# Kernel optimization log

Measured on AMD Instinct MI355X. Metric: run time of the kernel, lower is better.

Reference implementation:

```python
import jax, jax.numpy as jnp
import numpy as np
from jax import lax

EPS = 1e-5
NEG_SLOPE = 0.2


def inorm(x):
    # InstanceNorm3d (affine=False): per-sample, per-channel over spatial dims
    m = x.mean(axis=(2, 3, 4), keepdims=True)
    v = x.var(axis=(2, 3, 4), keepdims=True)
    return (x - m) * lax.rsqrt(v + EPS)


def lrelu(x):
    return jax.nn.leaky_relu(x, NEG_SLOPE)


def conv3d(x, w, b, pad, reflect=False):
    if pad > 0:
        mode = 'reflect' if reflect else 'constant'
        x = jnp.pad(x, ((0, 0), (0, 0), (pad, pad), (pad, pad), (pad, pad)), mode=mode)
    y = lax.conv_general_dilated(x, w, (1, 1, 1), 'VALID',
                                 dimension_numbers=('NCDHW', 'OIDHW', 'NCDHW'))
    return y + b[None, :, None, None, None]


def conv_block(x, w, b, pad):
    # ConvBlock: InstanceNorm -> LeakyReLU(0.2) -> Conv3d (reflect padding)
    return conv3d(lrelu(inorm(x)), w, b, pad, reflect=True)


def deform_conv3d(x, offset, w):
    # 3D deformable convolution, k=3, stride=1, pad=1, trilinear sampling, no bias
    B, C, H, W, D = x.shape
    K3 = 27
    off = offset.reshape(B, K3, 3, H, W, D)
    t = jnp.arange(3) - 1  # kernel taps relative to center (pad=1)
    tz, ty, tx = jnp.meshgrid(t, t, t, indexing='ij')
    taps = jnp.stack([tz, ty, tx], axis=-1).reshape(K3, 3).astype(x.dtype)
    gz, gy, gx = jnp.meshgrid(jnp.arange(H), jnp.arange(W), jnp.arange(D), indexing='ij')
    grid = jnp.stack([gz, gy, gx]).astype(x.dtype)  # [3,H,W,D]
    # sampling positions: [B,K3,3,H,W,D]
    pos = grid[None, None] + taps[None, :, :, None, None, None] + off
    p0 = jnp.floor(pos)
    frac = pos - p0
    p0i = p0.astype(jnp.int32)
    dims = jnp.array([H, W, D], dtype=jnp.int32)[None, None, :, None, None, None]
    xf = x.reshape(B, C, H * W * D)
    acc = jnp.zeros((B, C, K3, H * W * D), x.dtype)
    for dz in (0, 1):
        for dy in (0, 1):
            for dx in (0, 1):
                d = jnp.array([dz, dy, dx], dtype=jnp.int32)[None, None, :, None, None, None]
                idx = p0i + d  # [B,K3,3,H,W,D]
                valid = jnp.all((idx >= 0) & (idx < dims), axis=2)  # zero outside
                w3 = jnp.where(d == 1, frac, 1.0 - frac)
                wgt = w3.prod(axis=2) * valid.astype(x.dtype)  # [B,K3,H,W,D]
                ic = jnp.clip(idx, 0, dims - 1)
                flat = ((ic[:, :, 0] * W + ic[:, :, 1]) * D + ic[:, :, 2]).reshape(B, K3, -1)
                vals = jax.vmap(lambda xb, ib: xb[:, ib])(xf, flat)  # [B,C,K3,HWD]
                acc = acc + vals * wgt.reshape(B, 1, K3, -1)
    out = jnp.einsum('oik,bikp->bop', w.reshape(w.shape[0], w.shape[1], K3), acc)
    return out.reshape(B, -1, H, W, D)


def reference(x, w_first, b_first, w_na, b_na, w_last, b_last,
              w_fc1, b_fc1, w_fc2, b_fc2, w_off, b_off, w_def):
    B = x.shape[0]
    # SE-style channel-gated branch weights
    s = x.mean(axis=(2, 3, 4))                      # global avg pool -> [B,C]
    h = lrelu(s @ w_fc1.T + b_fc1)
    dw = jax.nn.softmax(h @ w_fc2.T + b_fc2, axis=1)  # [B,2]
    f = conv_block(x, w_first, b_first, pad=0)        # 1x1x1: 64 -> 32
    off = conv3d(f, w_off, b_off, pad=1, reflect=False)  # offsets [B,81,H,W,D]
    belta = deform_conv3d(f, off, w_def)
    alpha = conv_block(f, w_na, b_na, pad=1)
    comb = (belta * dw[:, 0][:, None, None, None, None]
            + alpha * dw[:, 1][:, None, None, None, None])
    return conv_block(comb, w_last, b_last, pad=0)


def setup_inputs() -> dict:
    key = jax.random.key(0)
    ks = jax.random.split(key, 16)
    C_in, C = 64, 32
    S = 32
    def rn(k, shape, scale):
        return jax.random.normal(k, shape, dtype=jnp.float32) * scale
    return {
        'x': rn(ks[0], (2, C_in, S, S, S), 1.0),
        'w_first': rn(ks[1], (C, C_in, 1, 1, 1), 0.05),
        'b_first': rn(ks[2], (C,), 0.05),
        'w_na': rn(ks[3], (C, C, 3, 3, 3), 0.05),
        'b_na': rn(ks[4], (C,), 0.05),
        'w_last': rn(ks[5], (C, C, 1, 1, 1), 0.05),
        'b_last': rn(ks[6], (C,), 0.05),
        'w_fc1': rn(ks[7], (16, C_in), 0.05),
        'b_fc1': rn(ks[8], (16,), 0.05),
        'w_fc2': rn(ks[9], (2, 16), 0.05),
        'b_fc2': rn(ks[10], (2,), 0.05),
        'w_off': rn(ks[11], (81, C, 3, 3, 3), 0.01),
        'b_off': jnp.zeros((81,), jnp.float32),
        'w_def': rn(ks[12], (C, C, 3, 3, 3), 0.05),
    }
```

## Files before the change

### kernel.cpp

```cpp
#include <hip/hip_runtime.h>
#include <hip/hip_bf16.h>

#define EPS 1e-5f

__global__ __launch_bounds__(256) void stats_kernel(
    const float* __restrict__ buf, float* __restrict__ mean,
    float* __restrict__ rstd) {
  int bc = blockIdx.x;
  const float* ch = buf + (size_t)bc * 32768;
  float s = 0.f, ss = 0.f;
  for (int i = threadIdx.x; i < 32768; i += 256) {
    float v = ch[i];
    s += v; ss += v * v;
  }
  for (int o = 32; o; o >>= 1) {
    s += __shfl_down(s, o);
    ss += __shfl_down(ss, o);
  }
  __shared__ float sb[4], ssb[4];
  int wid = threadIdx.x >> 6, lane = threadIdx.x & 63;
  if (lane == 0) { sb[wid] = s; ssb[wid] = ss; }
  __syncthreads();
  if (threadIdx.x == 0) {
    float S = 0.f, SS = 0.f;
    for (int w = 0; w < 4; ++w) { S += sb[w]; SS += ssb[w]; }
    float m = S * (1.f / 32768.f);
    float var = SS * (1.f / 32768.f) - m * m;
    mean[bc] = m;
    rstd[bc] = rsqrtf(var + EPS);
  }
}

__global__ void se_kernel(const float* __restrict__ mean_x,
                          const float* __restrict__ w1, const float* __restrict__ b1,
                          const float* __restrict__ w2, const float* __restrict__ b2,
                          float* __restrict__ dw) {
  __shared__ float hbuf[32];
  int t = threadIdx.x;
  if (t < 32) {
    int b = t >> 4, j = t & 15;
    float a = b1[j];
    for (int c = 0; c < 64; ++c) a += mean_x[b * 64 + c] * w1[j * 64 + c];
    hbuf[t] = a >= 0.f ? a : 0.2f * a;
  }
  __syncthreads();
  if (t < 2) {
    int b = t;
    float l0 = b2[0], l1 = b2[1];
    for (int j = 0; j < 16; ++j) {
      float h = hbuf[b * 16 + j];
      l0 += h * w2[j];
      l1 += h * w2[16 + j];
    }
    float m = fmaxf(l0, l1);
    float e0 = __expf(l0 - m), e1 = __expf(l1 - m);
    float inv = 1.f / (e0 + e1);
    dw[b * 2 + 0] = e0 * inv;
    dw[b * 2 + 1] = e1 * inv;
  }
}

__global__ __launch_bounds__(256) void prep_wdef(const float* __restrict__ w_def,
                                                 float* __restrict__ wTd) {
  int idx = blockIdx.x * 256 + threadIdx.x;
  if (idx < 27648) {
    int o = idx & 31, rest = idx >> 5;
    int i = rest & 31, k = rest >> 5;
    wTd[idx] = w_def[(size_t)(o * 32 + i) * 27 + k];
  }
}

__global__ __launch_bounds__(256) void prep_woff(const float* __restrict__ w_off,
                                                 float* __restrict__ wT) {
  int idx = blockIdx.x * 256 + threadIdx.x;
  if (idx < 69984) {
    int o = idx % 81, rest = idx / 81;
    int i = rest & 31, t = rest >> 5;
    wT[idx] = w_off[(size_t)(o * 32 + i) * 27 + t];
  }
}

__global__ __launch_bounds__(256) void prep_wna(const float* __restrict__ w_na,
                                                float* __restrict__ wT) {
  int idx = blockIdx.x * 256 + threadIdx.x;
  if (idx < 27648) {
    int o = idx & 31, rest = idx >> 5;
    int i = rest & 31, t = rest >> 5;
    wT[idx] = w_na[(size_t)(o * 32 + i) * 27 + t];
  }
}

__global__ __launch_bounds__(256) void first_conv_kernel(
    const float* __restrict__ x, const float* __restrict__ w,
    const float* __restrict__ bias,
    const float* __restrict__ meanp, const float* __restrict__ rstdp,
    float* __restrict__ f_cp, float* __restrict__ f_pc) {
  int og = blockIdx.x >> 8;
  int chunk = blockIdx.x & 255;
  int vg = chunk * 256 + threadIdx.x;
  int b = vg >> 15, p = vg & 32767;
  float acc[8];
#pragma unroll
  for (int o = 0; o < 8; ++o) acc[o] = 0.f;
  const float* xb = x + ((size_t)b * 64) * 32768;
  const float* wg = w + (size_t)og * 8 * 64;
  for (int i = 0; i < 64; ++i) {
    float v = xb[(size_t)i * 32768 + p];
    float m = meanp[b * 64 + i], r = rstdp[b * 64 + i];
    v = (v - m) * r;
    v = v >= 0.f ? v : 0.2f * v;
#pragma unroll
    for (int o = 0; o < 8; ++o) acc[o] = fmaf(wg[o * 64 + i], v, acc[o]);
  }
#pragma unroll
  for (int o = 0; o < 8; ++o) {
    acc[o] += bias[og * 8 + o];
    f_cp[((size_t)b * 32 + og * 8 + o) * 32768 + p] = acc[o];
  }
  float4 v0 = make_float4(acc[0], acc[1], acc[2], acc[3]);
  float4 v1 = make_float4(acc[4], acc[5], acc[6], acc[7]);
  float* pc = f_pc + ((size_t)b * 32768 + p) * 32 + og * 8;
  *(float4*)pc = v0;
  *(float4*)(pc + 4) = v1;
}

__global__ __launch_bounds__(256) void norm_f_kernel(
    const float* __restrict__ f_cp, const float* __restrict__ meanp,
    const float* __restrict__ rstdp, float* __restrict__ f_norm) {
  int i4 = blockIdx.x * 256 + threadIdx.x;
  int bc = (i4 * 4) >> 15;
  float m = meanp[bc], r = rstdp[bc];
  float4 v = ((const float4*)f_cp)[i4];
  float4 o;
  o.x = (v.x - m) * r; o.x = o.x >= 0.f ? o.x : 0.2f * o.x;
  o.y = (v.y - m) * r; o.y = o.y >= 0.f ? o.y : 0.2f * o.y;
  o.z = (v.z - m) * r; o.z = o.z >= 0.f ? o.z : 0.2f * o.z;
  o.w = (v.w - m) * r; o.w = o.w >= 0.f ? o.w : 0.2f * o.w;
  ((float4*)f_norm)[i4] = o;
}

template <int OCG, int OCT, bool REFLECT>
__global__ __launch_bounds__(256) void conv3_direct_kernel(
    const float* __restrict__ in,
    const float* __restrict__ wT,
    const float* __restrict__ bias,
    float* __restrict__ out) {
  int og = blockIdx.x >> 8;
  int chunk = blockIdx.x & 255;
  int vg = chunk * 256 + threadIdx.x;
  int b = vg >> 15, p = vg & 32767;
  int z = p >> 10, y = (p >> 5) & 31, x = p & 31;
  const float* base = in + ((size_t)b * 32) * 32768;

  float acc[OCG];
#pragma unroll
  for (int o = 0; o < OCG; ++o) acc[o] = 0.f;

  for (int t = 0; t < 27; ++t) {
    int dz = t / 9, dy = (t / 3) % 3, dx = t % 3;
    int zz = z + dz - 1, yy = y + dy - 1, xx = x + dx - 1;
    bool valid = true;
    if (REFLECT) {
      zz = zz < 0 ? -zz : (zz > 31 ? 62 - zz : zz);
      yy = yy < 0 ? -yy : (yy > 31 ? 62 - yy : yy);
      xx = xx < 0 ? -xx : (xx > 31 ? 62 - xx : xx);
    } else {
      valid = (unsigned)zz < 32u && (unsigned)yy < 32u && (unsigned)xx < 32u;
      if (!valid) { zz = 0; yy = 0; xx = 0; }
    }
    int off = (zz * 32 + yy) * 32 + xx;
    const float* cptr = base + off;
    const float* wt = wT + (size_t)t * 32 * OCT + og * OCG;
#pragma unroll 4
    for (int i = 0; i < 32; ++i) {
      float v = cptr[(size_t)i << 15];
      if (!REFLECT) v = valid ? v : 0.f;
#pragma unroll
      for (int o = 0; o < OCG; ++o)
        acc[o] = fmaf(wt[i * OCT + o], v, acc[o]);
    }
  }
  float* op = out + ((size_t)b * OCT + og * OCG) * 32768 + p;
#pragma unroll
  for (int o = 0; o < OCG; ++o)
    op[(size_t)o * 32768] = acc[o] + bias[og * OCG + o];
}

__global__ __launch_bounds__(256) void deform_kernel(
    const float* __restrict__ f_pc,
    const float* __restrict__ offs,
    const float* __restrict__ wTd,
    float* __restrict__ part) {
  int bid = blockIdx.x;
  int kg = bid >> 8;
  int tile = bid & 255;
  int vg = tile * 256 + threadIdx.x;
  int b = vg >> 15, p = vg & 32767;
  int z = p >> 10, y = (p >> 5) & 31, x = p & 31;
  const float* fb = f_pc + (((size_t)b) << 15) * 32;
  const float* ob = offs + (((size_t)b * 81) << 15);
  int kz = kg - 1;

  float acc[32];
#pragma unroll
  for (int o = 0; o < 32; ++o) acc[o] = 0.f;

  for (int kk = 0; kk < 9; ++kk) {
    int k = kg * 9 + kk;
    int ky = kk / 3 - 1, kx = kk % 3 - 1;

    float oz = ob[(size_t)(k * 3 + 0) * 32768 + p];
    float oy = ob[(size_t)(k * 3 + 1) * 32768 + p];
    float ox = ob[(size_t)(k * 3 + 2) * 32768 + p];
    float pz = (float)(z + kz) + oz;
    float py = (float)(y + ky) + oy;
    float px = (float)(x + kx) + ox;
    float fz = floorf(pz), fy = floorf(py), fxx = floorf(px);
    int iz0 = (int)fz, iy0 = (int)fy, ix0 = (int)fxx;
    float rz = pz - fz, ry = py - fy, rx = px - fxx;

    float v[32];
#pragma unroll
    for (int c = 0; c < 32; ++c) v[c] = 0.f;
#pragma unroll
    for (int corner = 0; corner < 8; ++corner) {
      int dz = corner >> 2, dy = (corner >> 1) & 1, dxx = corner & 1;
      int iz = iz0 + dz, iy = iy0 + dy, ix = ix0 + dxx;
      bool okb = (unsigned)iz < 32u && (unsigned)iy < 32u && (unsigned)ix < 32u;
      float wt = (dz ? rz : 1.f - rz) * (dy ? ry : 1.f - ry) *
                 (dxx ? rx : 1.f - rx);
      if (okb) {
        const float4* src =
            (const float4*)(fb + (size_t)((iz * 32 + iy) * 32 + ix) * 32);
#pragma unroll
        for (int q = 0; q < 8; ++q) {
          float4 u = src[q];
          v[q * 4 + 0] = fmaf(wt, u.x, v[q * 4 + 0]);
          v[q * 4 + 1] = fmaf(wt, u.y, v[q * 4 + 1]);
          v[q * 4 + 2] = fmaf(wt, u.z, v[q * 4 + 2]);
          v[q * 4 + 3] = fmaf(wt, u.w, v[q * 4 + 3]);
        }
      }
    }
    const float* wk = wTd + (size_t)k * 1024;
#pragma unroll
    for (int i = 0; i < 32; ++i) {
      float vi = v[i];
      const float* wr = wk + i * 32;
#pragma unroll
      for (int o = 0; o < 32; ++o) acc[o] = fmaf(wr[o], vi, acc[o]);
    }
  }
  float* obp = part + (((size_t)kg * 2 + b) * 32) * 32768 + p;
#pragma unroll
  for (int o = 0; o < 32; ++o) obp[(size_t)o * 32768] = acc[o];
}

__global__ __launch_bounds__(256) void combine_kernel(
    const float* __restrict__ part, const float* __restrict__ alpha,
    const float* __restrict__ dw, float* __restrict__ comb,
    float* __restrict__ partial) {
  int blk = blockIdx.x;
  int bc = blk >> 2, qt = blk & 3;
  int b = bc >> 5;
  float d0 = dw[b * 2 + 0], d1 = dw[b * 2 + 1];
  const float* p0 = part + (size_t)(bc) * 32768;
  const float* p1 = part + (size_t)(64 + bc) * 32768;
  const float* p2 = part + (size_t)(128 + bc) * 32768;
  const float* al = alpha + (size_t)bc * 32768;
  float* cb = comb + (size_t)bc * 32768;
  float s = 0.f, ss = 0.f;
  int i0 = qt * 8192;
  for (int i = i0 + threadIdx.x; i < i0 + 8192; i += 256) {
    float v = d0 * (p0[i] + p1[i] + p2[i]) + d1 * al[i];
    cb[i] = v;
    s += v; ss += v * v;
  }
  for (int o = 32; o; o >>= 1) {
    s += __shfl_down(s, o);
    ss += __shfl_down(ss, o);
  }
  __shared__ float sb[4], ssb[4];
  int wid = threadIdx.x >> 6, lane = threadIdx.x & 63;
  if (lane == 0) { sb[wid] = s; ssb[wid] = ss; }
  __syncthreads();
  if (threadIdx.x == 0) {
    float S = 0.f, SS = 0.f;
    for (int w = 0; w < 4; ++w) { S += sb[w]; SS += ssb[w]; }
    partial[blk * 2 + 0] = S;
    partial[blk * 2 + 1] = SS;
  }
}

__global__ void finalize_kernel(const float* __restrict__ partial,
                                float* __restrict__ mean, float* __restrict__ rstd) {
  int t = threadIdx.x;
  if (t < 64) {
    float S = 0.f, SS = 0.f;
    for (int q = 0; q < 4; ++q) {
      S += partial[(t * 4 + q) * 2 + 0];
      SS += partial[(t * 4 + q) * 2 + 1];
    }
    float m = S * (1.f / 32768.f);
    float var = SS * (1.f / 32768.f) - m * m;
    mean[t] = m;
    rstd[t] = rsqrtf(var + EPS);
  }
}

__global__ __launch_bounds__(256) void last_conv_kernel(
    const float* __restrict__ comb, const float* __restrict__ w,
    const float* __restrict__ bias,
    const float* __restrict__ meanp, const float* __restrict__ rstdp,
    float* __restrict__ out) {
  int og = blockIdx.x >> 8;
  int chunk = blockIdx.x & 255;
  int vg = chunk * 256 + threadIdx.x;
  int b = vg >> 15, p = vg & 32767;
  float acc[8];
#pragma unroll
  for (int o = 0; o < 8; ++o) acc[o] = 0.f;
  const float* cb = comb + ((size_t)b * 32) * 32768;
  const float* wg = w + (size_t)og * 8 * 32;
  for (int i = 0; i < 32; ++i) {
    float v = cb[(size_t)i * 32768 + p];
    float m = meanp[b * 32 + i], r = rstdp[b * 32 + i];
    v = (v - m) * r;
    v = v >= 0.f ? v : 0.2f * v;
#pragma unroll
    for (int o = 0; o < 8; ++o) acc[o] = fmaf(wg[o * 32 + i], v, acc[o]);
  }
#pragma unroll
  for (int o = 0; o < 8; ++o)
    out[((size_t)b * 32 + og * 8 + o) * 32768 + p] = acc[o] + bias[og * 8 + o];
}

extern "C" void kernel_launch(void* const* d_in, const int* in_sizes, int n_in,
                              void* d_out, int out_size, void* d_ws, size_t ws_size,
                              hipStream_t stream) {
  (void)in_sizes; (void)n_in; (void)out_size; (void)ws_size;
  const float* x       = (const float*)d_in[0];
  const float* w_first = (const float*)d_in[1];
  const float* b_first = (const float*)d_in[2];
  const float* w_na    = (const float*)d_in[3];
  const float* b_na    = (const float*)d_in[4];
  const float* w_last  = (const float*)d_in[5];
  const float* b_last  = (const float*)d_in[6];
  const float* w_fc1   = (const float*)d_in[7];
  const float* b_fc1   = (const float*)d_in[8];
  const float* w_fc2   = (const float*)d_in[9];
  const float* b_fc2   = (const float*)d_in[10];
  const float* w_off   = (const float*)d_in[11];
  const float* b_off   = (const float*)d_in[12];
  const float* w_def   = (const float*)d_in[13];
  float* out = (float*)d_out;

  float* ws = (float*)d_ws;
  float* mean_x  = ws + 0;
  float* rstd_x  = ws + 128;
  float* dwp     = ws + 256;
  float* mean_f  = ws + 272;
  float* rstd_f  = ws + 336;
  float* mean_c  = ws + 400;
  float* rstd_c  = ws + 464;
  float* partial = ws + 528;
  size_t off0 = 2048;
  float* wTd    = ws + off0;
  float* wT_off = wTd + 28672;
  float* wT_na  = wT_off + 71680;
  float* f_cp   = wT_na + 28672;
  float* f_pc   = f_cp + 2097152;
  float* offb   = f_pc + 2097152;
  float* alpha  = offb + 5308416;
  float* part   = alpha + 2097152;
  float* comb   = part + 6291456;
  float* f_norm = part;

  hipLaunchKernelGGL(stats_kernel, dim3(128), dim3(256), 0, stream, x, mean_x, rstd_x);
  hipLaunchKernelGGL(prep_wdef, dim3(108), dim3(256), 0, stream, w_def, wTd);
  hipLaunchKernelGGL(prep_woff, dim3(274), dim3(256), 0, stream, w_off, wT_off);
  hipLaunchKernelGGL(prep_wna, dim3(108), dim3(256), 0, stream, w_na, wT_na);
  hipLaunchKernelGGL(se_kernel, dim3(1), dim3(64), 0, stream,
                     mean_x, w_fc1, b_fc1, w_fc2, b_fc2, dwp);
  hipLaunchKernelGGL(first_conv_kernel, dim3(1024), dim3(256), 0, stream,
                     x, w_first, b_first, mean_x, rstd_x, f_cp, f_pc);
  hipLaunchKernelGGL(stats_kernel, dim3(64), dim3(256), 0, stream, f_cp, mean_f, rstd_f);
  hipLaunchKernelGGL(norm_f_kernel, dim3(2048), dim3(256), 0, stream,
                     f_cp, mean_f, rstd_f, f_norm);
  hipLaunchKernelGGL((conv3_direct_kernel<9, 81, false>), dim3(2304), dim3(256), 0, stream,
                     f_cp, wT_off, b_off, offb);
  hipLaunchKernelGGL((conv3_direct_kernel<8, 32, true>), dim3(1024), dim3(256), 0, stream,
                     f_norm, wT_na, b_na, alpha);
  hipLaunchKernelGGL(deform_kernel, dim3(768), dim3(256), 0, stream,
                     f_pc, offb, wTd, part);
  hipLaunchKernelGGL(combine_kernel, dim3(256), dim3(256), 0, stream,
                     part, alpha, dwp, comb, partial);
  hipLaunchKernelGGL(finalize_kernel, dim3(1), dim3(64), 0, stream,
                     partial, mean_c, rstd_c);
  hipLaunchKernelGGL(last_conv_kernel, dim3(1024), dim3(256), 0, stream,
                     comb, w_last, b_last, mean_c, rstd_c, out);
}
```

Measured before the change: 623.1 us.

## Gather deformable samples from channel-major features, dropping the point-major copy

```diff
diff --git a/kernel.cpp b/kernel.cpp
--- a/kernel.cpp
+++ b/kernel.cpp
@@ -94,7 +94,7 @@
     const float* __restrict__ x, const float* __restrict__ w,
     const float* __restrict__ bias,
     const float* __restrict__ meanp, const float* __restrict__ rstdp,
-    float* __restrict__ f_cp, float* __restrict__ f_pc) {
+    float* __restrict__ f_cp) {
   int og = blockIdx.x >> 8;
   int chunk = blockIdx.x & 255;
   int vg = chunk * 256 + threadIdx.x;
@@ -113,15 +113,8 @@
     for (int o = 0; o < 8; ++o) acc[o] = fmaf(wg[o * 64 + i], v, acc[o]);
   }
 #pragma unroll
-  for (int o = 0; o < 8; ++o) {
-    acc[o] += bias[og * 8 + o];
-    f_cp[((size_t)b * 32 + og * 8 + o) * 32768 + p] = acc[o];
-  }
-  float4 v0 = make_float4(acc[0], acc[1], acc[2], acc[3]);
-  float4 v1 = make_float4(acc[4], acc[5], acc[6], acc[7]);
-  float* pc = f_pc + ((size_t)b * 32768 + p) * 32 + og * 8;
-  *(float4*)pc = v0;
-  *(float4*)(pc + 4) = v1;
+  for (int o = 0; o < 8; ++o)
+    f_cp[((size_t)b * 32 + og * 8 + o) * 32768 + p] = acc[o] + bias[og * 8 + o];
 }
 
 __global__ __launch_bounds__(256) void norm_f_kernel(
@@ -187,7 +180,7 @@
 }
 
 __global__ __launch_bounds__(256) void deform_kernel(
-    const float* __restrict__ f_pc,
+    const float* __restrict__ f_cp,
     const float* __restrict__ offs,
     const float* __restrict__ wTd,
     float* __restrict__ part) {
@@ -197,7 +190,7 @@
   int vg = tile * 256 + threadIdx.x;
   int b = vg >> 15, p = vg & 32767;
   int z = p >> 10, y = (p >> 5) & 31, x = p & 31;
-  const float* fb = f_pc + (((size_t)b) << 15) * 32;
+  const float* fb = f_cp + ((size_t)b * 32) * 32768;
   const float* ob = offs + (((size_t)b * 81) << 15);
   int kz = kg - 1;
 
@@ -219,9 +212,8 @@
     int iz0 = (int)fz, iy0 = (int)fy, ix0 = (int)fxx;
     float rz = pz - fz, ry = py - fy, rx = px - fxx;
 
-    float v[32];
-#pragma unroll
-    for (int c = 0; c < 32; ++c) v[c] = 0.f;
+    int addr[8];
+    float wtm[8];
 #pragma unroll
     for (int corner = 0; corner < 8; ++corner) {
       int dz = corner >> 2, dy = (corner >> 1) & 1, dxx = corner & 1;
@@ -229,26 +221,19 @@
       bool okb = (unsigned)iz < 32u && (unsigned)iy < 32u && (unsigned)ix < 32u;
       float wt = (dz ? rz : 1.f - rz) * (dy ? ry : 1.f - ry) *
                  (dxx ? rx : 1.f - rx);
-      if (okb) {
-        const float4* src =
-            (const float4*)(fb + (size_t)((iz * 32 + iy) * 32 + ix) * 32);
-#pragma unroll
-        for (int q = 0; q < 8; ++q) {
-          float4 u = src[q];
-          v[q * 4 + 0] = fmaf(wt, u.x, v[q * 4 + 0]);
-          v[q * 4 + 1] = fmaf(wt, u.y, v[q * 4 + 1]);
-          v[q * 4 + 2] = fmaf(wt, u.z, v[q * 4 + 2]);
-          v[q * 4 + 3] = fmaf(wt, u.w, v[q * 4 + 3]);
-        }
-      }
-    }
-    const float* wk = wTd + (size_t)k * 1024;
-#pragma unroll
+      addr[corner] = okb ? (iz * 32 + iy) * 32 + ix : 0;
+      wtm[corner] = okb ? wt : 0.f;
+    }
+
+#pragma unroll 2
     for (int i = 0; i < 32; ++i) {
-      float vi = v[i];
-      const float* wr = wk + i * 32;
-#pragma unroll
-      for (int o = 0; o < 32; ++o) acc[o] = fmaf(wr[o], vi, acc[o]);
+      const float* ci = fb + ((size_t)i << 15);
+      float v = 0.f;
+#pragma unroll
+      for (int c = 0; c < 8; ++c) v = fmaf(wtm[c], ci[addr[c]], v);
+      const float* wr = wTd + ((size_t)k * 32 + i) * 32;
+#pragma unroll
+      for (int o = 0; o < 32; ++o) acc[o] = fmaf(wr[o], v, acc[o]);
     }
   }
   float* obp = part + (((size_t)kg * 2 + b) * 32) * 32768 + p;
@@ -383,7 +368,7 @@
   hipLaunchKernelGGL(se_kernel, dim3(1), dim3(64), 0, stream,
                      mean_x, w_fc1, b_fc1, w_fc2, b_fc2, dwp);
   hipLaunchKernelGGL(first_conv_kernel, dim3(1024), dim3(256), 0, stream,
-                     x, w_first, b_first, mean_x, rstd_x, f_cp, f_pc);
+                     x, w_first, b_first, mean_x, rstd_x, f_cp);
   hipLaunchKernelGGL(stats_kernel, dim3(64), dim3(256), 0, stream, f_cp, mean_f, rstd_f);
   hipLaunchKernelGGL(norm_f_kernel, dim3(2048), dim3(256), 0, stream,
                      f_cp, mean_f, rstd_f, f_norm);
@@ -392,7 +377,7 @@
   hipLaunchKernelGGL((conv3_direct_kernel<8, 32, true>), dim3(1024), dim3(256), 0, stream,
                      f_norm, wT_na, b_na, alpha);
   hipLaunchKernelGGL(deform_kernel, dim3(768), dim3(256), 0, stream,
-                     f_pc, offb, wTd, part);
+                     f_cp, offb, wTd, part);
   hipLaunchKernelGGL(combine_kernel, dim3(256), dim3(256), 0, stream,
                      part, alpha, dwp, comb, partial);
   hipLaunchKernelGGL(finalize_kernel, dim3(1), dim3(64), 0, stream,
```

After: 713.5 us. 1.15x slower.
